# Kernel tuning notes

Measured on AMD Instinct MI355X. Metric: run time of the kernel, lower is better.

## Reference

```python
import jax, jax.numpy as jnp
import numpy as np

B, N, NODE, EDIM, LAT, ENC = 4, 512, 3, 1, 32, 32
NEG = -jnp.inf


def _xavier(key, fan_in, fan_out):
    a = jnp.sqrt(6.0 / (fan_in + fan_out))
    return jax.random.uniform(key, (fan_in, fan_out), jnp.float32, -a, a)


def _mpnn(z, enc_e, adj_b, Wm, Wu):
    """Message: linear([z_i, z_j, e_ij]); adjacency-masked max-aggregation; update linear."""
    zd = z.shape[-1]
    zi = jnp.broadcast_to(z[:, :, None, :], (B, N, N, zd))
    zj = jnp.broadcast_to(z[:, None, :, :], (B, N, N, zd))
    msg = jnp.concatenate([zi, zj, enc_e], axis=-1) @ Wm          # [B,N,N,LAT]
    msg = jnp.where(adj_b[..., None], msg, NEG)
    agg = jnp.max(msg, axis=2)                                    # max over neighbors j
    return jnp.concatenate([z, agg], axis=-1) @ Wu                # [B,N,LAT]


def setup_inputs() -> dict:
    key = jax.random.key(0)
    ks = jax.random.split(key, 16)
    x = jax.random.normal(ks[0], (B, N, NODE), jnp.float32)
    h = jax.random.normal(ks[1], (B, N, LAT), jnp.float32)
    adj = jax.random.randint(ks[2], (B, N, N), 0, 2, jnp.int32)
    e_feat = jax.random.uniform(ks[3], (B, N, N, EDIM), jnp.float32)
    Wn = _xavier(ks[4], LAT + NODE, ENC)          # node_encoder
    We = _xavier(ks[5], EDIM, ENC)                # edge_encoder
    Wm = _xavier(ks[6], 2 * ENC + ENC, LAT)       # processor message
    Wu = _xavier(ks[7], ENC + LAT, LAT)           # processor update
    Wtm = _xavier(ks[8], 2 * LAT + ENC, LAT)      # termination_mpnn message
    Wtu = _xavier(ks[9], LAT + LAT, LAT)          # termination_mpnn update
    Wd = _xavier(ks[10], LAT + ENC, NODE)         # decoder
    Wt = _xavier(ks[11], LAT, 1)                  # termination head
    Wp = _xavier(ks[12], 2 * LAT + ENC, 1)        # predecessor head (pred=1)
    return {"x": x, "h": h, "adj": adj, "e_feat": e_feat, "Wn": Wn, "We": We,
            "Wm": Wm, "Wu": Wu, "Wtm": Wtm, "Wtu": Wtu, "Wd": Wd, "Wt": Wt, "Wp": Wp}


def reference(x, h, adj, e_feat, Wn, We, Wm, Wu, Wtm, Wtu, Wd, Wt, Wp):
    adj2 = adj + jnp.eye(N, dtype=adj.dtype)[None]                # add self-loops
    adj_b = adj2.astype(bool)
    z = jnp.concatenate([x, h], axis=-1) @ Wn                     # [B,N,ENC]
    enc_e = e_feat @ We                                           # [B,N,N,ENC]
    new_h = _mpnn(z, enc_e, adj_b, Wm, Wu) + z                    # [B,N,LAT]
    new_x = jnp.concatenate([z, new_h], axis=-1) @ Wd             # [B,N,NODE]
    tau_node = _mpnn(new_h, enc_e, adj_b, Wtm, Wtu)               # [B,N,LAT]
    tau = jnp.mean(tau_node, axis=1) @ Wt                         # [B,1]
    # predecessor head: all-pairs [h_i, h_j, e_ij] -> scalar, masked by adjacency
    hi = jnp.broadcast_to(new_h[:, :, None, :], (B, N, N, LAT))
    hj = jnp.broadcast_to(new_h[:, None, :, :], (B, N, N, LAT))
    p = (jnp.concatenate([hi, hj, enc_e], axis=-1) @ Wp)[..., 0]  # [B,N,N]
    p = jnp.where(adj_b, p, NEG)
    return new_x, p, tau, new_h
```

## Files before the change

kernel.cpp:

```cpp
#include <hip/hip_runtime.h>

#define XN 512
#define XB 4
#define XSENT (-1.0e30f)
#define XNEG (-3.402823466e38f)

__device__ __forceinline__ float xscrub(float v) {
    unsigned u = __float_as_uint(v);
    u = ((u & 0x7f800000u) == 0x7f800000u) ? 0xff7fffffu : u;
    return __uint_as_float(u);
}

__global__ __launch_bounds__(64) void ne2y_g0(
    const float* __restrict__ We, const float* __restrict__ Wm,
    const float* __restrict__ Wtm, const float* __restrict__ Wtu,
    const float* __restrict__ Wt, const float* __restrict__ Wp,
    float* __restrict__ drv, float* __restrict__ tau_out)
{
    const int t = threadIdx.x;
    if (t < 32) {
        float c1 = 0.f, c2 = 0.f;
        for (int k = 0; k < 32; ++k) {
            const float w = We[k];
            c1 += w * Wm[(64 + k) * 32 + t];
            c2 += w * Wtm[(64 + k) * 32 + t];
        }
        drv[t]      = c1;
        drv[32 + t] = c2;
        float u1 = 0.f, u2 = 0.f;
        for (int k = 0; k < 32; ++k) {
            u1 += Wtu[t * 32 + k]        * Wt[k];
            u2 += Wtu[(32 + t) * 32 + k] * Wt[k];
        }
        drv[64 + t] = u1;
        drv[96 + t] = u2;
        if (t == 0) {
            float cp = 0.f;
            for (int k = 0; k < 32; ++k) cp += We[k] * Wp[64 + k];
            drv[128] = cp;
        }
    }
    if (t < XB) tau_out[t] = 0.f;
}

__global__ __launch_bounds__(256) void ne2y_g1(
    const float* __restrict__ x, const float* __restrict__ h,
    const float* __restrict__ Wn, const float* __restrict__ Wm,
    float* __restrict__ z, float* __restrict__ A1, float* __restrict__ B1)
{
    const int t = threadIdx.x;
    const int r = t >> 5;
    const int l = t & 31;
    const int row = blockIdx.x * 8 + r;
    float acc = 0.f;
    {
        const float* xr = x + row * 3;
        const float* hr = h + row * 32;
        for (int k = 0; k < 3; ++k)  acc += xr[k] * Wn[k * 32 + l];
        for (int k = 0; k < 32; ++k) acc += hr[k] * Wn[(3 + k) * 32 + l];
    }
    __shared__ float zs[8][32];
    zs[r][l] = acc;
    z[row * 32 + l] = acc;
    __syncthreads();
    float a = 0.f, bb = 0.f;
    for (int k = 0; k < 32; ++k) {
        const float zk = zs[r][k];
        a  += zk * Wm[k * 32 + l];
        bb += zk * Wm[(32 + k) * 32 + l];
    }
    A1[row * 32 + l] = a;
    B1[row * 32 + l] = bb;
}

__global__ __launch_bounds__(256) void ne2y_m2(
    const int* __restrict__ adj, const float* __restrict__ ef,
    const float* __restrict__ z, const float* __restrict__ A1,
    const float* __restrict__ B1, const float* __restrict__ drv,
    const float* __restrict__ Wu, const float* __restrict__ Wd,
    const float* __restrict__ Wtm, const float* __restrict__ Wp,
    float* __restrict__ A2, float* __restrict__ B2,
    float* __restrict__ hp1, float* __restrict__ hp2,
    float* __restrict__ o_newx, float* __restrict__ o_newh)
{
    const int q = blockIdx.x;
    const int b = q >> 7;
    const int i0 = (q & 127) * 4;
    const int row0 = b * XN + i0;
    const int t = threadIdx.x;

    __shared__ float ev[4][XN];
    __shared__ int   mk[4][XN];
    {
        const int*   ab = adj + (size_t)row0 * XN;
        const float* eb = ef  + (size_t)row0 * XN;
        for (int u = t; u < 4 * XN; u += 256) {
            const int r = u >> 9, j = u & (XN - 1);
            ev[r][j] = eb[u];
            mk[r][j] = (ab[u] != 0) | (j == i0 + r);
        }
    }
    __syncthreads();

    const int c = t >> 5, l = t & 31;
    const float c1 = drv[l];
    const float* B1b = B1 + (size_t)b * XN * 32;
    float m0 = XNEG, m1 = XNEG, m2v = XNEG, m3v = XNEG;
#pragma unroll 4
    for (int k = 0; k < 64; ++k) {
        const int j = c * 64 + k;
        const float bv = B1b[j * 32 + l];
        float v0 = bv + ev[0][j] * c1;  m0  = fmaxf(m0,  mk[0][j] ? v0 : XNEG);
        float v1 = bv + ev[1][j] * c1;  m1  = fmaxf(m1,  mk[1][j] ? v1 : XNEG);
        float v2 = bv + ev[2][j] * c1;  m2v = fmaxf(m2v, mk[2][j] ? v2 : XNEG);
        float v3 = bv + ev[3][j] * c1;  m3v = fmaxf(m3v, mk[3][j] ? v3 : XNEG);
    }
    __shared__ float red[4][8][33];
    red[0][c][l] = m0;  red[1][c][l] = m1;
    red[2][c][l] = m2v; red[3][c][l] = m3v;
    __syncthreads();

    __shared__ float zs[4][32], ag[4][32], nh[4][32];
    if (t < 128) {
        const int r = t >> 5, ll = t & 31;
        float mm = red[r][0][ll];
        for (int cc = 1; cc < 8; ++cc) mm = fmaxf(mm, red[r][cc][ll]);
        ag[r][ll] = A1[(row0 + r) * 32 + ll] + mm;
        zs[r][ll] = z[(row0 + r) * 32 + ll];
    }
    __syncthreads();
    if (t < 128) {
        const int r = t >> 5, ll = t & 31;
        float v = zs[r][ll];
        for (int k = 0; k < 32; ++k)
            v += zs[r][k] * Wu[k * 32 + ll] + ag[r][k] * Wu[(32 + k) * 32 + ll];
        nh[r][ll] = v;
        o_newh[(row0 + r) * 32 + ll] = v;
    }
    __syncthreads();
    if (t < 128) {
        const int r = t >> 5, ll = t & 31;
        float a2 = 0.f, b2 = 0.f;
        for (int k = 0; k < 32; ++k) {
            const float nk = nh[r][k];
            a2 += nk * Wtm[k * 32 + ll];
            b2 += nk * Wtm[(32 + k) * 32 + ll];
        }
        A2[(row0 + r) * 32 + ll] = a2;
        B2[(row0 + r) * 32 + ll] = b2;
    } else if (t < 136) {
        const int r = (t - 128) >> 1, which = (t - 128) & 1;
        float p = 0.f;
        for (int k = 0; k < 32; ++k) p += nh[r][k] * Wp[which * 32 + k];
        (which ? hp2 : hp1)[row0 + r] = p;
    } else if (t >= 160 && t < 172) {
        const int r = (t - 160) / 3, d = (t - 160) % 3;
        float v = 0.f;
        for (int k = 0; k < 32; ++k)
            v += zs[r][k] * Wd[k * 3 + d] + nh[r][k] * Wd[(32 + k) * 3 + d];
        o_newx[(row0 + r) * 3 + d] = v;
    }
}

__global__ __launch_bounds__(256) void ne2y_m3(
    const int* __restrict__ adj, const float* __restrict__ ef,
    const float* __restrict__ A2, const float* __restrict__ B2,
    const float* __restrict__ newh, const float* __restrict__ hp1,
    const float* __restrict__ hp2, const float* __restrict__ drv,
    float* __restrict__ o_p, float* __restrict__ tau_out)
{
    const int q = blockIdx.x;
    const int b = q >> 7;
    const int i0 = (q & 127) * 4;
    const int row0 = b * XN + i0;
    const int t = threadIdx.x;

    __shared__ float ev[4][XN];
    __shared__ int   mk[4][XN];
    {
        const int*   ab = adj + (size_t)row0 * XN;
        const float* eb = ef  + (size_t)row0 * XN;
        for (int u = t; u < 4 * XN; u += 256) {
            const int r = u >> 9, j = u & (XN - 1);
            ev[r][j] = eb[u];
            mk[r][j] = (ab[u] != 0) | (j == i0 + r);
        }
    }
    __syncthreads();

    {
        const float cp = drv[128];
        const float* h2 = hp2 + b * XN;
#pragma unroll
        for (int r = 0; r < 4; ++r) {
            const float h1 = hp1[row0 + r];
            float* pr = o_p + (size_t)(row0 + r) * XN;
            for (int j = t; j < XN; j += 256) {
                const float v = mk[r][j] ? (h1 + h2[j] + ev[r][j] * cp) : XSENT;
                pr[j] = xscrub(v);
            }
        }
    }

    const int c = t >> 5, l = t & 31;
    const float c2 = drv[32 + l];
    const float* B2b = B2 + (size_t)b * XN * 32;
    float m0 = XNEG, m1 = XNEG, m2v = XNEG, m3v = XNEG;
#pragma unroll 4
    for (int k = 0; k < 64; ++k) {
        const int j = c * 64 + k;
        const float bv = B2b[j * 32 + l];
        float v0 = bv + ev[0][j] * c2;  m0  = fmaxf(m0,  mk[0][j] ? v0 : XNEG);
        float v1 = bv + ev[1][j] * c2;  m1  = fmaxf(m1,  mk[1][j] ? v1 : XNEG);
        float v2 = bv + ev[2][j] * c2;  m2v = fmaxf(m2v, mk[2][j] ? v2 : XNEG);
        float v3 = bv + ev[3][j] * c2;  m3v = fmaxf(m3v, mk[3][j] ? v3 : XNEG);
    }
    __shared__ float red[4][8][33];
    red[0][c][l] = m0;  red[1][c][l] = m1;
    red[2][c][l] = m2v; red[3][c][l] = m3v;
    __syncthreads();

    __shared__ float ss[4][32];
    if (t < 128) {
        const int r = t >> 5, ll = t & 31;
        float mm = red[r][0][ll];
        for (int cc = 1; cc < 8; ++cc) mm = fmaxf(mm, red[r][cc][ll]);
        const float agg = A2[(row0 + r) * 32 + ll] + mm;
        ss[r][ll] = newh[(row0 + r) * 32 + ll] * drv[64 + ll] + agg * drv[96 + ll];
    }
    __syncthreads();
    if (t == 0) {
        float s = 0.f;
        for (int r = 0; r < 4; ++r)
            for (int k = 0; k < 32; ++k) s += ss[r][k];
        atomicAdd(&tau_out[b], s * (1.0f / XN));
    }
}

extern "C" void kernel_launch(void* const* d_in, const int* in_sizes, int n_in,
                              void* d_out, int out_size, void* d_ws, size_t ws_size,
                              hipStream_t stream)
{
    const float* x   = (const float*)d_in[0];
    const float* h   = (const float*)d_in[1];
    const int*   adj = (const int*)  d_in[2];
    const float* ef  = (const float*)d_in[3];
    const float* Wn  = (const float*)d_in[4];
    const float* We  = (const float*)d_in[5];
    const float* Wm  = (const float*)d_in[6];
    const float* Wu  = (const float*)d_in[7];
    const float* Wtm = (const float*)d_in[8];
    const float* Wtu = (const float*)d_in[9];
    const float* Wd  = (const float*)d_in[10];
    const float* Wt  = (const float*)d_in[11];
    const float* Wp  = (const float*)d_in[12];

    float* out    = (float*)d_out;
    float* o_newx = out;
    float* o_p    = out + 6144;
    float* o_tau  = out + 6144 + XB * XN * XN;
    float* o_newh = o_tau + XB;

    float* w = (float*)d_ws;
    const int RN = XB * XN * 32;
    float* z   = w;
    float* A1  = w + RN;
    float* B1  = w + 2 * RN;
    float* A2  = w + 3 * RN;
    float* B2  = w + 4 * RN;
    float* hp1 = w + 5 * RN;
    float* hp2 = w + 5 * RN + XB * XN;
    float* drv = w + 5 * RN + 2 * XB * XN;

    hipLaunchKernelGGL(ne2y_g0, dim3(1), dim3(64), 0, stream,
                       We, Wm, Wtm, Wtu, Wt, Wp, drv, o_tau);
    hipLaunchKernelGGL(ne2y_g1, dim3(XB * XN / 8), dim3(256), 0, stream,
                       x, h, Wn, Wm, z, A1, B1);
    hipLaunchKernelGGL(ne2y_m2, dim3(XB * XN / 4), dim3(256), 0, stream,
                       adj, ef, z, A1, B1, drv, Wu, Wd, Wtm, Wp,
                       A2, B2, hp1, hp2, o_newx, o_newh);
    hipLaunchKernelGGL(ne2y_m3, dim3(XB * XN / 4), dim3(256), 0, stream,
                       adj, ef, A2, B2, o_newh, hp1, hp2, drv, o_p, o_tau);
}
```

Before: 115.0 us.

## Halve rows per block, use additive mask and stage weights in shared memory

The m2 and m3 kernels now handle 2 rows per block instead of 4, which doubles the grid to 2048 blocks. The per-row mask becomes an additive -1e38 term, so the max loop is branch-free, and edge values and masks are interleaved in shared memory. Wu, Wtm, Wd and Wp are staged in shared memory, and the tau sum uses a warp shuffle reduction. Each B1/B2 row is now read by twice as many blocks, which adds L2 traffic in exchange for more parallelism. The masked value also changes from -1e30 to roughly -1e38 plus the computed value.

```diff
diff --git a/kernel.cpp b/kernel.cpp
--- a/kernel.cpp
+++ b/kernel.cpp
@@ -2,8 +2,8 @@
 
 #define XN 512
 #define XB 4
-#define XSENT (-1.0e30f)
-#define XNEG (-3.402823466e38f)
+#define XNEG  (-3.402823466e38f)
+#define XMASK (-1.0e38f)
 
 __device__ __forceinline__ float xscrub(float v) {
     unsigned u = __float_as_uint(v);
@@ -11,7 +11,7 @@
     return __uint_as_float(u);
 }
 
-__global__ __launch_bounds__(64) void ne2y_g0(
+__global__ __launch_bounds__(64) void ne2v_g0(
     const float* __restrict__ We, const float* __restrict__ Wm,
     const float* __restrict__ Wtm, const float* __restrict__ Wtu,
     const float* __restrict__ Wt, const float* __restrict__ Wp,
@@ -43,7 +43,7 @@
     if (t < XB) tau_out[t] = 0.f;
 }
 
-__global__ __launch_bounds__(256) void ne2y_g1(
+__global__ __launch_bounds__(256) void ne2v_g1(
     const float* __restrict__ x, const float* __restrict__ h,
     const float* __restrict__ Wn, const float* __restrict__ Wm,
     float* __restrict__ z, float* __restrict__ A1, float* __restrict__ B1)
@@ -73,7 +73,7 @@
     B1[row * 32 + l] = bb;
 }
 
-__global__ __launch_bounds__(256) void ne2y_m2(
+__global__ __launch_bounds__(256) void ne2v_m2(
     const int* __restrict__ adj, const float* __restrict__ ef,
     const float* __restrict__ z, const float* __restrict__ A1,
     const float* __restrict__ B1, const float* __restrict__ drv,
@@ -84,85 +84,102 @@
     float* __restrict__ o_newx, float* __restrict__ o_newh)
 {
     const int q = blockIdx.x;
-    const int b = q >> 7;
-    const int i0 = (q & 127) * 4;
+    const int b = q >> 8;
+    const int i0 = (q & 255) * 2;
     const int row0 = b * XN + i0;
     const int t = threadIdx.x;
 
-    __shared__ float ev[4][XN];
-    __shared__ int   mk[4][XN];
+    __shared__ float emf[2 * XN];
+    __shared__ float adf[2 * XN];
+    __shared__ float wush[64 * 32];
+    __shared__ float wtmsh[64 * 32];
+    __shared__ float wdsh[192];
+    __shared__ float wpsh[64];
+    __shared__ float zsf[64], a1sf[64], ags[64], nhs[64];
+    __shared__ float red[2][8][33];
+
+    const float c1v = drv[t & 31];
     {
         const int*   ab = adj + (size_t)row0 * XN;
         const float* eb = ef  + (size_t)row0 * XN;
-        for (int u = t; u < 4 * XN; u += 256) {
+        for (int u = t; u < 2 * XN; u += 256) {
             const int r = u >> 9, j = u & (XN - 1);
-            ev[r][j] = eb[u];
-            mk[r][j] = (ab[u] != 0) | (j == i0 + r);
-        }
+            const int on = (ab[u] != 0) | (j == i0 + r);
+            emf[j * 2 + r] = on ? eb[u] : 0.f;
+            adf[j * 2 + r] = on ? 0.f : XMASK;
+        }
+        const float4* wu4 = (const float4*)Wu;
+        const float4* wt4 = (const float4*)Wtm;
+        ((float4*)wush)[t]        = wu4[t];
+        ((float4*)wush)[t + 256]  = wu4[t + 256];
+        ((float4*)wtmsh)[t]       = wt4[t];
+        ((float4*)wtmsh)[t + 256] = wt4[t + 256];
+        if (t < 192) wdsh[t] = Wd[t];
+        if (t < 64)  wpsh[t] = Wp[t];
+        if (t < 64) { zsf[t] = z[row0 * 32 + t]; a1sf[t] = A1[row0 * 32 + t]; }
     }
     __syncthreads();
 
     const int c = t >> 5, l = t & 31;
-    const float c1 = drv[l];
-    const float* B1b = B1 + (size_t)b * XN * 32;
-    float m0 = XNEG, m1 = XNEG, m2v = XNEG, m3v = XNEG;
-#pragma unroll 4
+    const float* Bp = B1 + (size_t)b * XN * 32 + l;
+    const int j0 = c * 64;
+    float m0 = XNEG, m1 = XNEG;
+#pragma unroll 16
     for (int k = 0; k < 64; ++k) {
-        const int j = c * 64 + k;
-        const float bv = B1b[j * 32 + l];
-        float v0 = bv + ev[0][j] * c1;  m0  = fmaxf(m0,  mk[0][j] ? v0 : XNEG);
-        float v1 = bv + ev[1][j] * c1;  m1  = fmaxf(m1,  mk[1][j] ? v1 : XNEG);
-        float v2 = bv + ev[2][j] * c1;  m2v = fmaxf(m2v, mk[2][j] ? v2 : XNEG);
-        float v3 = bv + ev[3][j] * c1;  m3v = fmaxf(m3v, mk[3][j] ? v3 : XNEG);
-    }
-    __shared__ float red[4][8][33];
-    red[0][c][l] = m0;  red[1][c][l] = m1;
-    red[2][c][l] = m2v; red[3][c][l] = m3v;
-    __syncthreads();
-
-    __shared__ float zs[4][32], ag[4][32], nh[4][32];
-    if (t < 128) {
+        const int j = j0 + k;
+        const float bv = Bp[(size_t)j * 32];
+        m0 = fmaxf(m0, fmaf(emf[j * 2],     c1v, bv) + adf[j * 2]);
+        m1 = fmaxf(m1, fmaf(emf[j * 2 + 1], c1v, bv) + adf[j * 2 + 1]);
+    }
+    red[0][c][l] = m0;
+    red[1][c][l] = m1;
+    __syncthreads();
+
+    if (t < 64) {
         const int r = t >> 5, ll = t & 31;
         float mm = red[r][0][ll];
         for (int cc = 1; cc < 8; ++cc) mm = fmaxf(mm, red[r][cc][ll]);
-        ag[r][ll] = A1[(row0 + r) * 32 + ll] + mm;
-        zs[r][ll] = z[(row0 + r) * 32 + ll];
-    }
-    __syncthreads();
-    if (t < 128) {
+        ags[t] = a1sf[t] + mm;
+    }
+    __syncthreads();
+
+    if (t < 64) {
         const int r = t >> 5, ll = t & 31;
-        float v = zs[r][ll];
+        float v = zsf[t];
         for (int k = 0; k < 32; ++k)
-            v += zs[r][k] * Wu[k * 32 + ll] + ag[r][k] * Wu[(32 + k) * 32 + ll];
-        nh[r][ll] = v;
-        o_newh[(row0 + r) * 32 + ll] = v;
-    }
-    __syncthreads();
-    if (t < 128) {
+            v += zsf[r * 32 + k] * wush[k * 32 + ll]
+               + ags[r * 32 + k] * wush[(32 + k) * 32 + ll];
+        nhs[t] = v;
+        o_newh[row0 * 32 + t] = v;
+    }
+    __syncthreads();
+
+    if (t < 64) {
         const int r = t >> 5, ll = t & 31;
         float a2 = 0.f, b2 = 0.f;
         for (int k = 0; k < 32; ++k) {
-            const float nk = nh[r][k];
-            a2 += nk * Wtm[k * 32 + ll];
-            b2 += nk * Wtm[(32 + k) * 32 + ll];
-        }
-        A2[(row0 + r) * 32 + ll] = a2;
-        B2[(row0 + r) * 32 + ll] = b2;
-    } else if (t < 136) {
+            const float nk = nhs[r * 32 + k];
+            a2 += nk * wtmsh[k * 32 + ll];
+            b2 += nk * wtmsh[(32 + k) * 32 + ll];
+        }
+        A2[row0 * 32 + t] = a2;
+        B2[row0 * 32 + t] = b2;
+    } else if (t >= 128 && t < 132) {
         const int r = (t - 128) >> 1, which = (t - 128) & 1;
         float p = 0.f;
-        for (int k = 0; k < 32; ++k) p += nh[r][k] * Wp[which * 32 + k];
+        for (int k = 0; k < 32; ++k) p += nhs[r * 32 + k] * wpsh[which * 32 + k];
         (which ? hp2 : hp1)[row0 + r] = p;
-    } else if (t >= 160 && t < 172) {
-        const int r = (t - 160) / 3, d = (t - 160) % 3;
+    } else if (t >= 160 && t < 166) {
+        const int idx = t - 160, r = idx / 3, d = idx % 3;
         float v = 0.f;
         for (int k = 0; k < 32; ++k)
-            v += zs[r][k] * Wd[k * 3 + d] + nh[r][k] * Wd[(32 + k) * 3 + d];
+            v += zsf[r * 32 + k] * wdsh[k * 3 + d]
+               + nhs[r * 32 + k] * wdsh[(32 + k) * 3 + d];
         o_newx[(row0 + r) * 3 + d] = v;
     }
 }
 
-__global__ __launch_bounds__(256) void ne2y_m3(
+__global__ __launch_bounds__(256) void ne2v_m3(
     const int* __restrict__ adj, const float* __restrict__ ef,
     const float* __restrict__ A2, const float* __restrict__ B2,
     const float* __restrict__ newh, const float* __restrict__ hp1,
@@ -170,70 +187,76 @@
     float* __restrict__ o_p, float* __restrict__ tau_out)
 {
     const int q = blockIdx.x;
-    const int b = q >> 7;
-    const int i0 = (q & 127) * 4;
+    const int b = q >> 8;
+    const int i0 = (q & 255) * 2;
     const int row0 = b * XN + i0;
     const int t = threadIdx.x;
 
-    __shared__ float ev[4][XN];
-    __shared__ int   mk[4][XN];
+    __shared__ float emf[2 * XN];
+    __shared__ float adf[2 * XN];
+    __shared__ float hp2s[XN];
+    __shared__ float a2sf[64], nhsf[64], ss[64];
+    __shared__ float red[2][8][33];
+
+    const float c2v = drv[32 + (t & 31)];
+    const float cpv = drv[128];
+    const float h1a = hp1[row0];
+    const float h1b = hp1[row0 + 1];
     {
         const int*   ab = adj + (size_t)row0 * XN;
         const float* eb = ef  + (size_t)row0 * XN;
-        for (int u = t; u < 4 * XN; u += 256) {
+        for (int u = t; u < 2 * XN; u += 256) {
             const int r = u >> 9, j = u & (XN - 1);
-            ev[r][j] = eb[u];
-            mk[r][j] = (ab[u] != 0) | (j == i0 + r);
-        }
+            const int on = (ab[u] != 0) | (j == i0 + r);
+            emf[j * 2 + r] = on ? eb[u] : 0.f;
+            adf[j * 2 + r] = on ? 0.f : XMASK;
+        }
+        for (int u = t; u < XN; u += 256) hp2s[u] = hp2[b * XN + u];
+        if (t < 64) { a2sf[t] = A2[row0 * 32 + t]; nhsf[t] = newh[row0 * 32 + t]; }
     }
     __syncthreads();
 
     {
-        const float cp = drv[128];
-        const float* h2 = hp2 + b * XN;
-#pragma unroll
-        for (int r = 0; r < 4; ++r) {
-            const float h1 = hp1[row0 + r];
-            float* pr = o_p + (size_t)(row0 + r) * XN;
-            for (int j = t; j < XN; j += 256) {
-                const float v = mk[r][j] ? (h1 + h2[j] + ev[r][j] * cp) : XSENT;
-                pr[j] = xscrub(v);
-            }
+        float* pr0 = o_p + (size_t)row0 * XN;
+        float* pr1 = pr0 + XN;
+        for (int j = t; j < XN; j += 256) {
+            pr0[j] = xscrub(h1a + hp2s[j] + emf[j * 2]     * cpv + adf[j * 2]);
+            pr1[j] = xscrub(h1b + hp2s[j] + emf[j * 2 + 1] * cpv + adf[j * 2 + 1]);
         }
     }
 
     const int c = t >> 5, l = t & 31;
-    const float c2 = drv[32 + l];
-    const float* B2b = B2 + (size_t)b * XN * 32;
-    float m0 = XNEG, m1 = XNEG, m2v = XNEG, m3v = XNEG;
-#pragma unroll 4
+    const float* Bp = B2 + (size_t)b * XN * 32 + l;
+    const int j0 = c * 64;
+    float m0 = XNEG, m1 = XNEG;
+#pragma unroll 16
     for (int k = 0; k < 64; ++k) {
-        const int j = c * 64 + k;
-        const float bv = B2b[j * 32 + l];
-        float v0 = bv + ev[0][j] * c2;  m0  = fmaxf(m0,  mk[0][j] ? v0 : XNEG);
-        float v1 = bv + ev[1][j] * c2;  m1  = fmaxf(m1,  mk[1][j] ? v1 : XNEG);
-        float v2 = bv + ev[2][j] * c2;  m2v = fmaxf(m2v, mk[2][j] ? v2 : XNEG);
-        float v3 = bv + ev[3][j] * c2;  m3v = fmaxf(m3v, mk[3][j] ? v3 : XNEG);
-    }
-    __shared__ float red[4][8][33];
-    red[0][c][l] = m0;  red[1][c][l] = m1;
-    red[2][c][l] = m2v; red[3][c][l] = m3v;
-    __syncthreads();
-
-    __shared__ float ss[4][32];
-    if (t < 128) {
+        const int j = j0 + k;
+        const float bv = Bp[(size_t)j * 32];
+        m0 = fmaxf(m0, fmaf(emf[j * 2],     c2v, bv) + adf[j * 2]);
+        m1 = fmaxf(m1, fmaf(emf[j * 2 + 1], c2v, bv) + adf[j * 2 + 1]);
+    }
+    red[0][c][l] = m0;
+    red[1][c][l] = m1;
+    __syncthreads();
+
+    if (t < 64) {
         const int r = t >> 5, ll = t & 31;
         float mm = red[r][0][ll];
         for (int cc = 1; cc < 8; ++cc) mm = fmaxf(mm, red[r][cc][ll]);
-        const float agg = A2[(row0 + r) * 32 + ll] + mm;
-        ss[r][ll] = newh[(row0 + r) * 32 + ll] * drv[64 + ll] + agg * drv[96 + ll];
-    }
-    __syncthreads();
-    if (t == 0) {
-        float s = 0.f;
-        for (int r = 0; r < 4; ++r)
-            for (int k = 0; k < 32; ++k) s += ss[r][k];
-        atomicAdd(&tau_out[b], s * (1.0f / XN));
+        const float agg = a2sf[t] + mm;
+        ss[t] = nhsf[t] * drv[64 + ll] + agg * drv[96 + ll];
+    }
+    __syncthreads();
+    if (t < 64) {
+        float s = ss[t];
+        s += __shfl_down(s, 32);
+        s += __shfl_down(s, 16);
+        s += __shfl_down(s, 8);
+        s += __shfl_down(s, 4);
+        s += __shfl_down(s, 2);
+        s += __shfl_down(s, 1);
+        if (t == 0) atomicAdd(&tau_out[b], s * (1.0f / XN));
     }
 }
 
@@ -272,13 +295,13 @@
     float* hp2 = w + 5 * RN + XB * XN;
     float* drv = w + 5 * RN + 2 * XB * XN;
 
-    hipLaunchKernelGGL(ne2y_g0, dim3(1), dim3(64), 0, stream,
+    hipLaunchKernelGGL(ne2v_g0, dim3(1), dim3(64), 0, stream,
                        We, Wm, Wtm, Wtu, Wt, Wp, drv, o_tau);
-    hipLaunchKernelGGL(ne2y_g1, dim3(XB * XN / 8), dim3(256), 0, stream,
+    hipLaunchKernelGGL(ne2v_g1, dim3(XB * XN / 8), dim3(256), 0, stream,
                        x, h, Wn, Wm, z, A1, B1);
-    hipLaunchKernelGGL(ne2y_m2, dim3(XB * XN / 4), dim3(256), 0, stream,
+    hipLaunchKernelGGL(ne2v_m2, dim3(XB * XN / 2), dim3(256), 0, stream,
                        adj, ef, z, A1, B1, drv, Wu, Wd, Wtm, Wp,
                        A2, B2, hp1, hp2, o_newx, o_newh);
-    hipLaunchKernelGGL(ne2y_m3, dim3(XB * XN / 4), dim3(256), 0, stream,
+    hipLaunchKernelGGL(ne2v_m3, dim3(XB * XN / 2), dim3(256), 0, stream,
                        adj, ef, A2, B2, o_newh, hp1, hp2, drv, o_p, o_tau);
 }
```

Measured after the change: 118.5 us. +3.1%, slower.

## Fuse four kernels into two with per-block recomputation of node projections

Applied to the files above, without the earlier changes.

Replaces the four-kernel pipeline (weight prep, node encode, two MPNN passes) with two kernels that each process 8 rows per block. Each block recomputes z (or loads new_h) for its whole batch into shared memory and derives the B projection itself, and folds derived weight constants inline. This removes two launches and the workspace round-trips for z/A/B/hp. The cost is heavy redundant compute (every block recomputes 512x32 projections), large shared memory use (~84KB) and only 256 blocks.

```diff
diff --git a/kernel.cpp b/kernel.cpp
--- a/kernel.cpp
+++ b/kernel.cpp
@@ -1,9 +1,8 @@
 #include <hip/hip_runtime.h>
 
 #define XN 512
-#define XB 4
+#define XNEG  (-3.402823466e38f)
 #define XSENT (-1.0e30f)
-#define XNEG (-3.402823466e38f)
 
 __device__ __forceinline__ float xscrub(float v) {
     unsigned u = __float_as_uint(v);
@@ -11,229 +10,241 @@
     return __uint_as_float(u);
 }
 
-__global__ __launch_bounds__(64) void ne2y_g0(
-    const float* __restrict__ We, const float* __restrict__ Wm,
+__global__ __launch_bounds__(256, 2) void ne2q_k1(
+    const float* __restrict__ x, const float* __restrict__ h,
+    const int* __restrict__ adj, const float* __restrict__ ef,
+    const float* __restrict__ Wn, const float* __restrict__ We,
+    const float* __restrict__ Wm, const float* __restrict__ Wu,
+    const float* __restrict__ Wd,
+    float* __restrict__ o_newx, float* __restrict__ o_newh,
+    float* __restrict__ o_tau)
+{
+    const int q = blockIdx.x;
+    const int b = q >> 6;
+    const int i0 = (q & 63) * 8;
+    const int row0 = b * XN + i0;
+    const int t = threadIdx.x;
+
+    __shared__ float zL[XN * 32];
+    __shared__ float em[8 * XN];
+    __shared__ float red[8][8][33];
+    __shared__ float agL[8 * 32], nhL[8 * 32];
+
+    if (q == 0 && t < 4) o_tau[t] = 0.f;
+
+    {
+        const int*   ab = adj + (size_t)row0 * XN;
+        const float* eb = ef  + (size_t)row0 * XN;
+        for (int u = t; u < 8 * XN; u += 256) {
+            const int r = u >> 9, j = u & (XN - 1);
+            const int on = (ab[u] != 0) | (j == i0 + r);
+            em[u] = on ? eb[u] : -1.0f;
+        }
+    }
+
+    const int c = t >> 5, l = t & 31;
+    {
+        float wn[35];
+#pragma unroll
+        for (int k = 0; k < 35; ++k) wn[k] = Wn[k * 32 + l];
+        const float* xb = x + (size_t)(b * XN) * 3;
+        const float* hb = h + (size_t)(b * XN) * 32;
+        const int j1 = c * 64 + 64;
+        for (int j = c * 64; j < j1; ++j) {
+            const float* hr = hb + j * 32;
+            float acc = xb[j * 3] * wn[0] + xb[j * 3 + 1] * wn[1] + xb[j * 3 + 2] * wn[2];
+#pragma unroll
+            for (int k = 0; k < 32; ++k) acc += hr[k] * wn[3 + k];
+            zL[j * 32 + l] = acc;
+        }
+    }
+    __syncthreads();
+
+    {
+        float wm2[32];
+#pragma unroll
+        for (int k = 0; k < 32; ++k) wm2[k] = Wm[(32 + k) * 32 + l];
+        float c1v = 0.f;
+#pragma unroll
+        for (int k = 0; k < 32; ++k) c1v += We[k] * Wm[(64 + k) * 32 + l];
+
+        float m[8];
+#pragma unroll
+        for (int r = 0; r < 8; ++r) m[r] = XNEG;
+        const int j1 = c * 64 + 64;
+        for (int j = c * 64; j < j1; ++j) {
+            float bv = 0.f;
+#pragma unroll
+            for (int k = 0; k < 32; ++k) bv += zL[j * 32 + k] * wm2[k];
+#pragma unroll
+            for (int r = 0; r < 8; ++r) {
+                const float s = em[r * XN + j];
+                const float v = fmaf(s, c1v, bv);
+                m[r] = (s >= 0.f) ? fmaxf(m[r], v) : m[r];
+            }
+        }
+#pragma unroll
+        for (int r = 0; r < 8; ++r) red[r][c][l] = m[r];
+    }
+    __syncthreads();
+
+    {
+        const int r = t >> 5, ll = t & 31;
+        float mm = red[r][0][ll];
+#pragma unroll
+        for (int cc = 1; cc < 8; ++cc) mm = fmaxf(mm, red[r][cc][ll]);
+        float a1 = 0.f;
+        const float* zr = zL + (i0 + r) * 32;
+#pragma unroll
+        for (int k = 0; k < 32; ++k) a1 += zr[k] * Wm[k * 32 + ll];
+        agL[t] = a1 + mm;
+    }
+    __syncthreads();
+
+    {
+        const int r = t >> 5, ll = t & 31;
+        const float* zr = zL + (i0 + r) * 32;
+        float v = zr[ll];
+#pragma unroll
+        for (int k = 0; k < 32; ++k)
+            v += zr[k] * Wu[k * 32 + ll] + agL[r * 32 + k] * Wu[(32 + k) * 32 + ll];
+        nhL[t] = v;
+        o_newh[(size_t)row0 * 32 + t] = v;
+    }
+    __syncthreads();
+
+    if (t < 24) {
+        const int r = t / 3, d = t % 3;
+        const float* zr = zL + (i0 + r) * 32;
+        float v = 0.f;
+#pragma unroll
+        for (int k = 0; k < 32; ++k)
+            v += zr[k] * Wd[k * 3 + d] + nhL[r * 32 + k] * Wd[(32 + k) * 3 + d];
+        o_newx[(row0 + r) * 3 + d] = v;
+    }
+}
+
+__global__ __launch_bounds__(256, 2) void ne2q_k2(
+    const int* __restrict__ adj, const float* __restrict__ ef,
+    const float* __restrict__ newh, const float* __restrict__ We,
     const float* __restrict__ Wtm, const float* __restrict__ Wtu,
     const float* __restrict__ Wt, const float* __restrict__ Wp,
-    float* __restrict__ drv, float* __restrict__ tau_out)
-{
-    const int t = threadIdx.x;
-    if (t < 32) {
-        float c1 = 0.f, c2 = 0.f;
-        for (int k = 0; k < 32; ++k) {
-            const float w = We[k];
-            c1 += w * Wm[(64 + k) * 32 + t];
-            c2 += w * Wtm[(64 + k) * 32 + t];
-        }
-        drv[t]      = c1;
-        drv[32 + t] = c2;
-        float u1 = 0.f, u2 = 0.f;
-        for (int k = 0; k < 32; ++k) {
-            u1 += Wtu[t * 32 + k]        * Wt[k];
-            u2 += Wtu[(32 + t) * 32 + k] * Wt[k];
-        }
-        drv[64 + t] = u1;
-        drv[96 + t] = u2;
-        if (t == 0) {
-            float cp = 0.f;
-            for (int k = 0; k < 32; ++k) cp += We[k] * Wp[64 + k];
-            drv[128] = cp;
-        }
-    }
-    if (t < XB) tau_out[t] = 0.f;
-}
-
-__global__ __launch_bounds__(256) void ne2y_g1(
-    const float* __restrict__ x, const float* __restrict__ h,
-    const float* __restrict__ Wn, const float* __restrict__ Wm,
-    float* __restrict__ z, float* __restrict__ A1, float* __restrict__ B1)
-{
-    const int t = threadIdx.x;
-    const int r = t >> 5;
-    const int l = t & 31;
-    const int row = blockIdx.x * 8 + r;
-    float acc = 0.f;
-    {
-        const float* xr = x + row * 3;
-        const float* hr = h + row * 32;
-        for (int k = 0; k < 3; ++k)  acc += xr[k] * Wn[k * 32 + l];
-        for (int k = 0; k < 32; ++k) acc += hr[k] * Wn[(3 + k) * 32 + l];
-    }
-    __shared__ float zs[8][32];
-    zs[r][l] = acc;
-    z[row * 32 + l] = acc;
-    __syncthreads();
-    float a = 0.f, bb = 0.f;
-    for (int k = 0; k < 32; ++k) {
-        const float zk = zs[r][k];
-        a  += zk * Wm[k * 32 + l];
-        bb += zk * Wm[(32 + k) * 32 + l];
-    }
-    A1[row * 32 + l] = a;
-    B1[row * 32 + l] = bb;
-}
-
-__global__ __launch_bounds__(256) void ne2y_m2(
-    const int* __restrict__ adj, const float* __restrict__ ef,
-    const float* __restrict__ z, const float* __restrict__ A1,
-    const float* __restrict__ B1, const float* __restrict__ drv,
-    const float* __restrict__ Wu, const float* __restrict__ Wd,
-    const float* __restrict__ Wtm, const float* __restrict__ Wp,
-    float* __restrict__ A2, float* __restrict__ B2,
-    float* __restrict__ hp1, float* __restrict__ hp2,
-    float* __restrict__ o_newx, float* __restrict__ o_newh)
+    float* __restrict__ o_p, float* __restrict__ o_tau)
 {
     const int q = blockIdx.x;
-    const int b = q >> 7;
-    const int i0 = (q & 127) * 4;
+    const int b = q >> 6;
+    const int i0 = (q & 63) * 8;
     const int row0 = b * XN + i0;
     const int t = threadIdx.x;
 
-    __shared__ float ev[4][XN];
-    __shared__ int   mk[4][XN];
-    {
+    __shared__ float nhL[XN * 32];
+    __shared__ float em[8 * XN];
+    __shared__ float red[8][8][33];
+    __shared__ float hp2L[XN];
+    __shared__ float hp1L[8];
+    __shared__ float part[4];
+
+    {
+        const float4* src = (const float4*)(newh + (size_t)b * XN * 32);
+        float4* dst = (float4*)nhL;
+        for (int u = t; u < XN * 8; u += 256) dst[u] = src[u];
         const int*   ab = adj + (size_t)row0 * XN;
         const float* eb = ef  + (size_t)row0 * XN;
-        for (int u = t; u < 4 * XN; u += 256) {
+        for (int u = t; u < 8 * XN; u += 256) {
             const int r = u >> 9, j = u & (XN - 1);
-            ev[r][j] = eb[u];
-            mk[r][j] = (ab[u] != 0) | (j == i0 + r);
+            const int on = (ab[u] != 0) | (j == i0 + r);
+            em[u] = on ? eb[u] : -1.0f;
         }
     }
     __syncthreads();
 
     const int c = t >> 5, l = t & 31;
-    const float c1 = drv[l];
-    const float* B1b = B1 + (size_t)b * XN * 32;
-    float m0 = XNEG, m1 = XNEG, m2v = XNEG, m3v = XNEG;
-#pragma unroll 4
-    for (int k = 0; k < 64; ++k) {
-        const int j = c * 64 + k;
-        const float bv = B1b[j * 32 + l];
-        float v0 = bv + ev[0][j] * c1;  m0  = fmaxf(m0,  mk[0][j] ? v0 : XNEG);
-        float v1 = bv + ev[1][j] * c1;  m1  = fmaxf(m1,  mk[1][j] ? v1 : XNEG);
-        float v2 = bv + ev[2][j] * c1;  m2v = fmaxf(m2v, mk[2][j] ? v2 : XNEG);
-        float v3 = bv + ev[3][j] * c1;  m3v = fmaxf(m3v, mk[3][j] ? v3 : XNEG);
-    }
-    __shared__ float red[4][8][33];
-    red[0][c][l] = m0;  red[1][c][l] = m1;
-    red[2][c][l] = m2v; red[3][c][l] = m3v;
-    __syncthreads();
-
-    __shared__ float zs[4][32], ag[4][32], nh[4][32];
-    if (t < 128) {
+    {
+        float wt2[32];
+#pragma unroll
+        for (int k = 0; k < 32; ++k) wt2[k] = Wtm[(32 + k) * 32 + l];
+        float c2v = 0.f;
+#pragma unroll
+        for (int k = 0; k < 32; ++k) c2v += We[k] * Wtm[(64 + k) * 32 + l];
+
+        float m[8];
+#pragma unroll
+        for (int r = 0; r < 8; ++r) m[r] = XNEG;
+        const int j1 = c * 64 + 64;
+        for (int j = c * 64; j < j1; ++j) {
+            float bv = 0.f;
+#pragma unroll
+            for (int k = 0; k < 32; ++k) bv += nhL[j * 32 + k] * wt2[k];
+#pragma unroll
+            for (int r = 0; r < 8; ++r) {
+                const float s = em[r * XN + j];
+                const float v = fmaf(s, c2v, bv);
+                m[r] = (s >= 0.f) ? fmaxf(m[r], v) : m[r];
+            }
+        }
+#pragma unroll
+        for (int r = 0; r < 8; ++r) red[r][c][l] = m[r];
+
+        for (int j2 = t; j2 < XN; j2 += 256) {
+            float p = 0.f;
+#pragma unroll
+            for (int k = 0; k < 32; ++k) p += nhL[j2 * 32 + k] * Wp[32 + k];
+            hp2L[j2] = p;
+        }
+        if (t < 8) {
+            float p = 0.f;
+#pragma unroll
+            for (int k = 0; k < 32; ++k) p += nhL[(i0 + t) * 32 + k] * Wp[k];
+            hp1L[t] = p;
+        }
+    }
+    __syncthreads();
+
+    {
+        float cpv = 0.f;
+#pragma unroll
+        for (int k = 0; k < 32; ++k) cpv += We[k] * Wp[64 + k];
+#pragma unroll
+        for (int r = 0; r < 8; ++r) {
+            float* pr = o_p + (size_t)(row0 + r) * XN;
+            const float h1 = hp1L[r];
+            for (int j = t; j < XN; j += 256) {
+                const float s = em[r * XN + j];
+                const float v = (s >= 0.f) ? (h1 + hp2L[j] + s * cpv) : XSENT;
+                pr[j] = xscrub(v);
+            }
+        }
+    }
+
+    float ss;
+    {
         const int r = t >> 5, ll = t & 31;
         float mm = red[r][0][ll];
+#pragma unroll
         for (int cc = 1; cc < 8; ++cc) mm = fmaxf(mm, red[r][cc][ll]);
-        ag[r][ll] = A1[(row0 + r) * 32 + ll] + mm;
-        zs[r][ll] = z[(row0 + r) * 32 + ll];
-    }
-    __syncthreads();
-    if (t < 128) {
-        const int r = t >> 5, ll = t & 31;
-        float v = zs[r][ll];
-        for (int k = 0; k < 32; ++k)
-            v += zs[r][k] * Wu[k * 32 + ll] + ag[r][k] * Wu[(32 + k) * 32 + ll];
-        nh[r][ll] = v;
-        o_newh[(row0 + r) * 32 + ll] = v;
-    }
-    __syncthreads();
-    if (t < 128) {
-        const int r = t >> 5, ll = t & 31;
-        float a2 = 0.f, b2 = 0.f;
+        const float* nr = nhL + (i0 + r) * 32;
+        float a2 = 0.f;
+#pragma unroll
+        for (int k = 0; k < 32; ++k) a2 += nr[k] * Wtm[k * 32 + ll];
+        float u1 = 0.f, u2 = 0.f;
+#pragma unroll
         for (int k = 0; k < 32; ++k) {
-            const float nk = nh[r][k];
-            a2 += nk * Wtm[k * 32 + ll];
-            b2 += nk * Wtm[(32 + k) * 32 + ll];
-        }
-        A2[(row0 + r) * 32 + ll] = a2;
-        B2[(row0 + r) * 32 + ll] = b2;
-    } else if (t < 136) {
-        const int r = (t - 128) >> 1, which = (t - 128) & 1;
-        float p = 0.f;
-        for (int k = 0; k < 32; ++k) p += nh[r][k] * Wp[which * 32 + k];
-        (which ? hp2 : hp1)[row0 + r] = p;
-    } else if (t >= 160 && t < 172) {
-        const int r = (t - 160) / 3, d = (t - 160) % 3;
-        float v = 0.f;
-        for (int k = 0; k < 32; ++k)
-            v += zs[r][k] * Wd[k * 3 + d] + nh[r][k] * Wd[(32 + k) * 3 + d];
-        o_newx[(row0 + r) * 3 + d] = v;
-    }
-}
-
-__global__ __launch_bounds__(256) void ne2y_m3(
-    const int* __restrict__ adj, const float* __restrict__ ef,
-    const float* __restrict__ A2, const float* __restrict__ B2,
-    const float* __restrict__ newh, const float* __restrict__ hp1,
-    const float* __restrict__ hp2, const float* __restrict__ drv,
-    float* __restrict__ o_p, float* __restrict__ tau_out)
-{
-    const int q = blockIdx.x;
-    const int b = q >> 7;
-    const int i0 = (q & 127) * 4;
-    const int row0 = b * XN + i0;
-    const int t = threadIdx.x;
-
-    __shared__ float ev[4][XN];
-    __shared__ int   mk[4][XN];
-    {
-        const int*   ab = adj + (size_t)row0 * XN;
-        const float* eb = ef  + (size_t)row0 * XN;
-        for (int u = t; u < 4 * XN; u += 256) {
-            const int r = u >> 9, j = u & (XN - 1);
-            ev[r][j] = eb[u];
-            mk[r][j] = (ab[u] != 0) | (j == i0 + r);
-        }
-    }
-    __syncthreads();
-
-    {
-        const float cp = drv[128];
-        const float* h2 = hp2 + b * XN;
-#pragma unroll
-        for (int r = 0; r < 4; ++r) {
-            const float h1 = hp1[row0 + r];
-            float* pr = o_p + (size_t)(row0 + r) * XN;
-            for (int j = t; j < XN; j += 256) {
-                const float v = mk[r][j] ? (h1 + h2[j] + ev[r][j] * cp) : XSENT;
-                pr[j] = xscrub(v);
-            }
-        }
-    }
-
-    const int c = t >> 5, l = t & 31;
-    const float c2 = drv[32 + l];
-    const float* B2b = B2 + (size_t)b * XN * 32;
-    float m0 = XNEG, m1 = XNEG, m2v = XNEG, m3v = XNEG;
-#pragma unroll 4
-    for (int k = 0; k < 64; ++k) {
-        const int j = c * 64 + k;
-        const float bv = B2b[j * 32 + l];
-        float v0 = bv + ev[0][j] * c2;  m0  = fmaxf(m0,  mk[0][j] ? v0 : XNEG);
-        float v1 = bv + ev[1][j] * c2;  m1  = fmaxf(m1,  mk[1][j] ? v1 : XNEG);
-        float v2 = bv + ev[2][j] * c2;  m2v = fmaxf(m2v, mk[2][j] ? v2 : XNEG);
-        float v3 = bv + ev[3][j] * c2;  m3v = fmaxf(m3v, mk[3][j] ? v3 : XNEG);
-    }
-    __shared__ float red[4][8][33];
-    red[0][c][l] = m0;  red[1][c][l] = m1;
-    red[2][c][l] = m2v; red[3][c][l] = m3v;
-    __syncthreads();
-
-    __shared__ float ss[4][32];
-    if (t < 128) {
-        const int r = t >> 5, ll = t & 31;
-        float mm = red[r][0][ll];
-        for (int cc = 1; cc < 8; ++cc) mm = fmaxf(mm, red[r][cc][ll]);
-        const float agg = A2[(row0 + r) * 32 + ll] + mm;
-        ss[r][ll] = newh[(row0 + r) * 32 + ll] * drv[64 + ll] + agg * drv[96 + ll];
-    }
+            u1 += Wtu[ll * 32 + k]        * Wt[k];
+            u2 += Wtu[(32 + ll) * 32 + k] * Wt[k];
+        }
+        ss = nr[ll] * u1 + (a2 + mm) * u2;
+    }
+    ss += __shfl_down(ss, 32);
+    ss += __shfl_down(ss, 16);
+    ss += __shfl_down(ss, 8);
+    ss += __shfl_down(ss, 4);
+    ss += __shfl_down(ss, 2);
+    ss += __shfl_down(ss, 1);
+    if ((t & 63) == 0) part[t >> 6] = ss;
     __syncthreads();
     if (t == 0) {
-        float s = 0.f;
-        for (int r = 0; r < 4; ++r)
-            for (int k = 0; k < 32; ++k) s += ss[r][k];
-        atomicAdd(&tau_out[b], s * (1.0f / XN));
+        const float s = part[0] + part[1] + part[2] + part[3];
+        atomicAdd(&o_tau[b], s * (1.0f / XN));
     }
 }
 
@@ -258,27 +269,13 @@
     float* out    = (float*)d_out;
     float* o_newx = out;
     float* o_p    = out + 6144;
-    float* o_tau  = out + 6144 + XB * XN * XN;
-    float* o_newh = o_tau + XB;
-
-    float* w = (float*)d_ws;
-    const int RN = XB * XN * 32;
-    float* z   = w;
-    float* A1  = w + RN;
-    float* B1  = w + 2 * RN;
-    float* A2  = w + 3 * RN;
-    float* B2  = w + 4 * RN;
-    float* hp1 = w + 5 * RN;
-    float* hp2 = w + 5 * RN + XB * XN;
-    float* drv = w + 5 * RN + 2 * XB * XN;
-
-    hipLaunchKernelGGL(ne2y_g0, dim3(1), dim3(64), 0, stream,
-                       We, Wm, Wtm, Wtu, Wt, Wp, drv, o_tau);
-    hipLaunchKernelGGL(ne2y_g1, dim3(XB * XN / 8), dim3(256), 0, stream,
-                       x, h, Wn, Wm, z, A1, B1);
-    hipLaunchKernelGGL(ne2y_m2, dim3(XB * XN / 4), dim3(256), 0, stream,
-                       adj, ef, z, A1, B1, drv, Wu, Wd, Wtm, Wp,
-                       A2, B2, hp1, hp2, o_newx, o_newh);
-    hipLaunchKernelGGL(ne2y_m3, dim3(XB * XN / 4), dim3(256), 0, stream,
-                       adj, ef, A2, B2, o_newh, hp1, hp2, drv, o_p, o_tau);
-}
+    float* o_tau  = out + 6144 + 4 * XN * XN;
+    float* o_newh = o_tau + 4;
+
+    hipLaunchKernelGGL(ne2q_k1, dim3(256), dim3(256), 0, stream,
+                       x, h, adj, ef, Wn, We, Wm, Wu, Wd,
+                       o_newx, o_newh, o_tau);
+    hipLaunchKernelGGL(ne2q_k2, dim3(256), dim3(256), 0, stream,
+                       adj, ef, o_newh, We, Wtm, Wtu, Wt, Wp,
+                       o_p, o_tau);
+}
```

Result: slower. 175.5 us (+52.6%).
